# Optimization experiments

Measured on AMD Instinct MI355X. Metric: run time of the kernel, lower is better.

The kernel has to match this reference:

```python
import jax, jax.numpy as jnp
import numpy as np
import math

HEAD_NUM = 16


def _split_qkv(qkv, head_num):
    # torch: rearrange(qkv, 'b t (d k h) -> k b h t d', k=3, h=head_num)
    B, T, E3 = qkv.shape
    d = E3 // (3 * head_num)
    qkv = qkv.reshape(B, T, d, 3, head_num)        # (b,t,d,k,h)
    qkv = jnp.transpose(qkv, (3, 0, 4, 1, 2))       # (k,b,h,t,d)
    return qkv[0], qkv[1], qkv[2]


def setup_inputs() -> dict:
    key = jax.random.key(0)
    ks = jax.random.split(key, 6)
    B, T, E = 4, 1024, 1024
    return {
        "x": jax.random.normal(ks[0], (B, T, E), dtype=jnp.float32),
        "y": jax.random.normal(ks[1], (B, T, E), dtype=jnp.float32),
        "Wqkv1": jax.random.normal(ks[2], (3 * E, E), dtype=jnp.float32) * 0.02,
        "Wqkv2": jax.random.normal(ks[3], (3 * E, E), dtype=jnp.float32) * 0.02,
        "Wout1": jax.random.normal(ks[4], (E, E), dtype=jnp.float32) * 0.02,
        "Wout2": jax.random.normal(ks[5], (E, E), dtype=jnp.float32) * 0.02,
    }


def reference(x, y, Wqkv1, Wqkv2, Wout1, Wout2):
    B, T, E = x.shape
    H = HEAD_NUM
    dk = math.sqrt(E / H)

    qkv1 = x @ Wqkv1.T                              # (B,T,3E)
    qkv2 = y @ Wqkv2.T
    q1, k1, v1 = _split_qkv(qkv1, H)                # each (B,H,T,d)
    q2, k2, v2 = _split_qkv(qkv2, H)

    # cross attention: stream-2 queries attend to stream-1 keys/values and vice versa
    energy1 = jnp.einsum('bhid,bhjd->bhij', q2, k1) / dk
    energy2 = jnp.einsum('bhid,bhjd->bhij', q1, k2) / dk
    attn1 = jax.nn.softmax(energy1, axis=-1)
    attn2 = jax.nn.softmax(energy2, axis=-1)

    xo = jnp.einsum('bhij,bhjd->bhid', attn1, v1)   # (B,H,T,d)
    yo = jnp.einsum('bhij,bhjd->bhid', attn2, v2)
    xo = jnp.transpose(xo, (0, 2, 1, 3)).reshape(B, T, E)  # b t (h d)
    yo = jnp.transpose(yo, (0, 2, 1, 3)).reshape(B, T, E)

    return xo @ Wout1.T, yo @ Wout2.T
```

## Files before the change

kernel.cpp:

```cpp
#include <hip/hip_runtime.h>
#include <hip/hip_bf16.h>

typedef __hip_bfloat16 bf16;
typedef __attribute__((ext_vector_type(8))) short short8;
typedef __attribute__((ext_vector_type(4))) short short4v;
typedef __attribute__((ext_vector_type(4))) float f32x4;

#define MFMA_BF16(a, b, c) __builtin_amdgcn_mfma_f32_16x16x32_bf16((a), (b), (c), 0, 0, 0)

#define QSCALE 0.1803368860111270f

__device__ __forceinline__ short f2bf(float f) {
    union { bf16 h; short s; } u;
    u.h = __float2bfloat16(f);
    return u.s;
}

#if defined(__has_builtin) && __has_builtin(__builtin_amdgcn_cvt_pk_bf16_f32)
typedef __attribute__((ext_vector_type(2))) __bf16 bf16x2_t;
__device__ __forceinline__ unsigned int pk2(float a, float b) {
    union { bf16x2_t v; unsigned int u; } x;
    x.v = __builtin_amdgcn_cvt_pk_bf16_f32(a, b);
    return x.u;
}
#else
__device__ __forceinline__ unsigned int pk2(float a, float b) {
    union { bf16 h[2]; unsigned int u; } x;
    x.h[0] = __float2bfloat16(a);
    x.h[1] = __float2bfloat16(b);
    return x.u;
}
#endif

#if defined(__has_builtin) && __has_builtin(__builtin_amdgcn_exp2f)
#define EXP2F(x) __builtin_amdgcn_exp2f(x)
#else
#define EXP2F(x) exp2f(x)
#endif

__device__ __forceinline__ void gload16(const void* g, void* l) {
    __builtin_amdgcn_global_load_lds(
        (const __attribute__((address_space(1))) unsigned int*)g,
        (__attribute__((address_space(3))) unsigned int*)l, 16, 0, 0);
}

__global__ void cvt_fused(const float* __restrict__ x, const float* __restrict__ y,
                          const float* __restrict__ wo1, const float* __restrict__ wo2,
                          const float* __restrict__ wq1, const float* __restrict__ wq2,
                          bf16* __restrict__ ox, bf16* __restrict__ oy,
                          bf16* __restrict__ oo1, bf16* __restrict__ oo2,
                          bf16* __restrict__ oq1, bf16* __restrict__ oq2) {
    const int yb = blockIdx.y;
    if (yb < 4) {
        int i = blockIdx.x * 256 + threadIdx.x;
        const float* src; bf16* dst; int n4;
        switch (yb) {
            case 0:  src = x;   dst = ox;  n4 = 1048576; break;
            case 1:  src = y;   dst = oy;  n4 = 1048576; break;
            case 2:  src = wo1; dst = oo1; n4 = 262144;  break;
            default: src = wo2; dst = oo2; n4 = 262144;  break;
        }
        if (i >= n4) return;
        float4 f = reinterpret_cast<const float4*>(src)[i];
        short4v s;
        s.x = f2bf(f.x); s.y = f2bf(f.y); s.z = f2bf(f.z); s.w = f2bf(f.w);
        reinterpret_cast<short4v*>(dst)[i] = s;
    } else {
        const int np = blockIdx.x;
        if (np >= 3072) return;
        const int comp = np >> 10, rem = np & 1023, h = rem >> 6, d = rem & 63;
        const int srow = d * 48 + comp * 16 + h;
        const float* src = ((yb == 5) ? wq2 : wq1) + (long)srow * 1024;
        bf16* dst = ((yb == 5) ? oq2 : oq1) + (long)np * 1024;
        const float sc = (comp == 0) ? QSCALE : 1.0f;
        int t = threadIdx.x;
        float4 f = reinterpret_cast<const float4*>(src)[t];
        short4v s;
        s.x = f2bf(f.x * sc); s.y = f2bf(f.y * sc); s.z = f2bf(f.z * sc); s.w = f2bf(f.w * sc);
        reinterpret_cast<short4v*>(dst)[t] = s;
    }
}

__global__ __launch_bounds__(512, 4)
void gemm_qkv128(const bf16* __restrict__ A0g, const bf16* __restrict__ B0g,
                 void* o0a, void* o0b, void* o0c,
                 const bf16* __restrict__ A1g, const bf16* __restrict__ B1g,
                 void* o1a, void* o1b, void* o1c) {
    extern __shared__ short smem[];
    const int z = blockIdx.z;
    const short* A = reinterpret_cast<const short*>(z ? A1g : A0g);
    const short* B = reinterpret_cast<const short*>(z ? B1g : B0g);
    const int tid  = threadIdx.x;
    const int lane = tid & 63;
    const int w    = tid >> 6;
    const int quad = lane >> 4;
    const int l16  = lane & 15;
    const long M0 = (long)blockIdx.y * 128;
    const long N0 = (long)blockIdx.x * 256;

    const int wm = w >> 2;
    const int wn = w & 3;
    const int cA0  = (quad ^ ((l16 >> 1) & 3)) * 8;
    const int aoff = wm * 2048 + l16 * 32;
    const int boff = 4096 + wn * 1024 + l16 * 32;

    const int srow = lane >> 2;
    const int scs  = ((lane & 3) ^ ((srow >> 1) & 3)) * 8;
    const short* Asrc = A + (M0 + 16 * w + srow) * 1024 + scs;
    const short* Bsrc = B + (N0 + 32 * w + srow) * 1024 + scs;

    f32x4 acc[2][4][2] = {};
    short8 af[4], bfv[2];

#define SA128(tt, nbase) do { \
    gload16(Asrc + (tt) * 32, smem + (nbase) + w * 512); } while (0)
#define SB128(tt, nbase) do { \
    const short* _s = Bsrc + (tt) * 32; \
    short* _d = smem + (nbase) + 4096 + w * 1024; \
    gload16(_s, _d); gload16(_s + 16384, _d + 512); } while (0)
#define RDA128(bbv) do { \
    _Pragma("unroll") for (int mt = 0; mt < 4; ++mt) \
        af[mt] = *reinterpret_cast<const short8*>(&smem[(bbv) + aoff + mt * 512 + cA0]); } while (0)
#define RDB128(Bh, bbv) do { \
    _Pragma("unroll") for (int nt = 0; nt < 2; ++nt) \
        bfv[nt] = *reinterpret_cast<const short8*>(&smem[(bbv) + (Bh) * 4096 + boff + nt * 512 + cA0]); } while (0)
#define MM128(p) do { \
    __builtin_amdgcn_s_setprio(1); \
    _Pragma("unroll") for (int mt = 0; mt < 4; ++mt) \
    _Pragma("unroll") for (int nt = 0; nt < 2; ++nt) \
        acc[p][mt][nt] = MFMA_BF16(af[mt], bfv[nt], acc[p][mt][nt]); \
    __builtin_amdgcn_s_setprio(0); } while (0)

    SA128(0, 0); SB128(0, 0);

    int bcur = 0;
#pragma unroll 1
    for (int t = 0; t < 32; ++t) {
        int bnext = bcur + 1; if (bnext == 3) bnext = 0;
        if (t < 31) {
            const int nb = bnext * 12288;
            SA128(t + 1, nb); SB128(t + 1, nb);
            asm volatile("s_waitcnt vmcnt(3)" ::: "memory");
        } else {
            asm volatile("s_waitcnt vmcnt(0)" ::: "memory");
        }
        __builtin_amdgcn_s_barrier();
        __builtin_amdgcn_sched_barrier(0);

        const int bb = bcur * 12288;
        RDA128(bb);
        RDB128(0, bb);
        MM128(0);
        RDB128(1, bb);
        MM128(1);
        bcur = bnext;
    }

    __syncthreads();

    if (blockIdx.x < 8) {
        short* dst = reinterpret_cast<short*>(blockIdx.x < 4 ? (z ? o1a : o0a)
                                                             : (z ? o1b : o0b));
        const int b = (int)(M0 >> 10);
        const int t00 = ((int)M0 & 1023) + wm * 64 + quad * 4;
        const int hd00 = ((int)blockIdx.x & 3) * 256 + wn * 32;
#pragma unroll
        for (int Bh = 0; Bh < 2; ++Bh)
#pragma unroll
            for (int nt = 0; nt < 2; ++nt) {
                const int hd = hd00 + Bh * 128 + nt * 16 + l16;
                const int h = hd >> 6, d = hd & 63;
                short* dp = dst + (long)(b * 16 + h) * 65536 + d;
#pragma unroll
                for (int mt = 0; mt < 4; ++mt)
#pragma unroll
                    for (int r = 0; r < 4; ++r)
                        dp[(long)(t00 + mt * 16 + r) * 64] = f2bf(acc[Bh][mt][nt][r]);
            }
    } else {
        short* vT = reinterpret_cast<short*>(z ? o1c : o0c);
        const int b = (int)(M0 >> 10);
        const int hd00 = ((int)blockIdx.x - 8) * 256 + wn * 32;
        short* ws = smem + w * 2304;
        const int c8 = (lane & 7) * 8;
        const int colr = lane >> 3;
        const int tb = ((int)M0 & 1023) + wm * 64 + c8;
#pragma unroll
        for (int Bh = 0; Bh < 2; ++Bh) {
#pragma unroll
            for (int nt = 0; nt < 2; ++nt)
#pragma unroll
                for (int mt = 0; mt < 4; ++mt) {
                    uint2 uu;
                    uu.x = pk2(acc[Bh][mt][nt][0], acc[Bh][mt][nt][1]);
                    uu.y = pk2(acc[Bh][mt][nt][2], acc[Bh][mt][nt][3]);
                    *reinterpret_cast<uint2*>(&ws[(nt * 16 + l16) * 72 + mt * 16 + quad * 4]) = uu;
                }
#pragma unroll
            for (int q4 = 0; q4 < 4; ++q4) {
                const int col = q4 * 8 + colr;
                const int hd = hd00 + Bh * 128 + col;
                const int h = hd >> 6, d = hd & 63;
                short8 v = *reinterpret_cast<const short8*>(&ws[col * 72 + c8]);
                *reinterpret_cast<short8*>(&vT[(long)(b * 16 + h) * 65536 + (long)d * 1024 + tb]) = v;
            }
        }
    }
#undef SA128
#undef SB128
#undef RDA128
#undef RDB128
#undef MM128
}

__global__ __launch_bounds__(256)
void gemm_out(const bf16* __restrict__ A0g, const bf16* __restrict__ B0g, float* __restrict__ C0,
              const bf16* __restrict__ A1g, const bf16* __restrict__ B1g, float* __restrict__ C1) {
    __shared__ short smem2[24576];
    const int z = blockIdx.z;
    const short* A = reinterpret_cast<const short*>(z ? A1g : A0g);
    const short* B = reinterpret_cast<const short*>(z ? B1g : B0g);
    const int tid  = threadIdx.x;
    const int lane = tid & 63;
    const int w    = tid >> 6;
    const int wr   = w >> 1;
    const int wc   = w & 1;
    const int quad = lane >> 4;
    const int l16  = lane & 15;
    const long bM = (long)blockIdx.y * 128;

    f32x4 acc[4][4] = {};

    const int sr  = lane >> 2;
    const int scs = ((lane & 3) ^ (sr & 3)) * 8;
    const short* Ag0 = A + (bM + 32 * w + sr) * 1024 + scs;
    const short* Ag1 = Ag0 + 16 * 1024;
    const short* Bg0 = B + ((long)blockIdx.x * 128 + 32 * w + sr) * 1024 + scs;
    const short* Bg1 = Bg0 + 16 * 1024;
    const int sq = (quad ^ (l16 & 3)) * 8;

    {
        short* sb = smem2;
        gload16(Ag0, sb + w * 1024);
        gload16(Ag1, sb + w * 1024 + 512);
        gload16(Bg0, sb + 4096 + w * 1024);
        gload16(Bg1, sb + 4096 + w * 1024 + 512);
    }

    int bcur = 0;
#pragma unroll 1
    for (int iter = 0; iter < 32; ++iter) {
        int bnext = bcur + 1; if (bnext == 3) bnext = 0;
        if (iter < 31) {
            const int koff = (iter + 1) * 32;
            short* sb = smem2 + bnext * 8192;
            gload16(Ag0 + koff, sb + w * 1024);
            gload16(Ag1 + koff, sb + w * 1024 + 512);
            gload16(Bg0 + koff, sb + 4096 + w * 1024);
            gload16(Bg1 + koff, sb + 4096 + w * 1024 + 512);
            asm volatile("s_waitcnt vmcnt(4)" ::: "memory");
        } else {
            asm volatile("s_waitcnt vmcnt(0)" ::: "memory");
        }
        __builtin_amdgcn_s_barrier();
        __builtin_amdgcn_sched_barrier(0);

        const short* Ab = smem2 + bcur * 8192;
        const short* Bb = Ab + 4096;

        short8 af[4], bfr[4];
#pragma unroll
        for (int mt = 0; mt < 4; ++mt)
            af[mt] = *reinterpret_cast<const short8*>(&Ab[(wr * 64 + mt * 16 + l16) * 32 + sq]);
#pragma unroll
        for (int nt = 0; nt < 4; ++nt)
            bfr[nt] = *reinterpret_cast<const short8*>(&Bb[(wc * 64 + nt * 16 + l16) * 32 + sq]);
        __builtin_amdgcn_s_setprio(1);
#pragma unroll
        for (int mt = 0; mt < 4; ++mt)
#pragma unroll
            for (int nt = 0; nt < 4; ++nt)
                acc[mt][nt] = MFMA_BF16(af[mt], bfr[nt], acc[mt][nt]);
        __builtin_amdgcn_s_setprio(0);
        bcur = bnext;
    }

    float* C = z ? C1 : C0;
    const long crow = bM + wr * 64 + quad * 4;
    const long ccol = (long)blockIdx.x * 128 + wc * 64 + l16;
#pragma unroll
    for (int mt = 0; mt < 4; ++mt)
#pragma unroll
        for (int nt = 0; nt < 4; ++nt)
#pragma unroll
            for (int r = 0; r < 4; ++r)
                C[(crow + mt * 16 + r) * 1024L + ccol + nt * 16] = acc[mt][nt][r];
}

__global__ __launch_bounds__(256)
void attn_kernel(const bf16* __restrict__ q0g, const bf16* __restrict__ k0g,
                 const bf16* __restrict__ v0g, bf16* __restrict__ o0g,
                 const bf16* __restrict__ q1g, const bf16* __restrict__ k1g,
                 const bf16* __restrict__ v1g, bf16* __restrict__ o1g) {
    __shared__ short smem[24576];
    const int bh = blockIdx.x;
    const int qt = blockIdx.y;
    const int z = blockIdx.z;
    const int b = bh >> 4, h = bh & 15;
    const int tid = threadIdx.x, lane = tid & 63, w = tid >> 6;
    const int quad = lane >> 4, l16 = lane & 15;

    const short* Qb = reinterpret_cast<const short*>(z ? q1g : q0g) + (long)bh * 1024 * 64;
    const short* Kb = reinterpret_cast<const short*>(z ? k1g : k0g) + (long)bh * 1024 * 64;
    const short* Vb = reinterpret_cast<const short*>(z ? v1g : v0g) + (long)bh * 64 * 1024;
    short* Ob = reinterpret_cast<short*>(z ? o1g : o0g);

    short8 qb[2][2];
#pragma unroll
    for (int qg = 0; qg < 2; ++qg) {
        const short* Qp = Qb + (long)(qt * 128 + qg * 64 + w * 16 + l16) * 64;
        qb[qg][0] = *reinterpret_cast<const short8*>(Qp + quad * 8);
        qb[qg][1] = *reinterpret_cast<const short8*>(Qp + 32 + quad * 8);
    }

    const int r8  = lane >> 3;
    const int sc0 = ((lane & 7) ^ (r8 & 3)) * 8;
    const short* Kg0 = Kb + (long)(16 * w + r8) * 64 + sc0;
    const short* Kg1 = Kb + (long)(16 * w + 8 + r8) * 64 + (sc0 ^ 32);
    const short* Vg0 = Vb + (long)(16 * w + r8) * 1024 + sc0;
    const short* Vg1 = Vb + (long)(16 * w + 8 + r8) * 1024 + (sc0 ^ 32);

    const int jbase = 8 * (l16 >> 2) + (l16 & 3);
    const int fKs = (l16 & 3) | (((l16 >> 2) & 1) << 2);
    const int s0  = (quad ^ fKs) * 8;
    const int fVs = (l16 & 3) | (((l16 >> 3) & 1) << 2);
    const int sv  = (quad ^ fVs) * 8;

    f32x4 o[2][4] = {};
    float li[2] = {0.f, 0.f};

    gload16(Kg0, smem + w * 1024); gload16(Kg1, smem + w * 1024 + 512);
    gload16(Vg0, smem + 4096 + w * 1024); gload16(Vg1, smem + 4096 + w * 1024 + 512);

    int bcur = 0;
#pragma unroll 1
    for (int iter = 0; iter < 16; ++iter) {
        int bnext = bcur + 1; if (bnext == 3) bnext = 0;
        if (iter < 15) {
            short* sb = smem + bnext * 8192;
            const long ko = (long)(iter + 1) * 4096;
            const long vo = (long)(iter + 1) * 64;
            gload16(Kg0 + ko, sb + w * 1024);
            gload16(Kg1 + ko, sb + w * 1024 + 512);
            gload16(Vg0 + vo, sb + 4096 + w * 1024);
            gload16(Vg1 + vo, sb + 4096 + w * 1024 + 512);
            asm volatile("s_waitcnt vmcnt(4)" ::: "memory");
        } else {
            asm volatile("s_waitcnt vmcnt(0)" ::: "memory");
        }
        __builtin_amdgcn_s_barrier();
        __builtin_amdgcn_sched_barrier(0);

        const short* Ks = smem + bcur * 8192;
        const short* Vs = Ks + 4096;

        f32x4 st[2][4];
        __builtin_amdgcn_s_setprio(1);
#pragma unroll
        for (int g = 0; g < 4; ++g) {
            const int goff = (g >> 1) * 32 + (g & 1) * 4;
            const short* kr = Ks + (jbase + goff) * 64;
            short8 k0 = *reinterpret_cast<const short8*>(kr + s0);
            short8 k1 = *reinterpret_cast<const short8*>(kr + (s0 ^ 32));
#pragma unroll
            for (int qg = 0; qg < 2; ++qg) {
                f32x4 zf = {0.f, 0.f, 0.f, 0.f};
                zf = MFMA_BF16(k0, qb[qg][0], zf);
                zf = MFMA_BF16(k1, qb[qg][1], zf);
                st[qg][g] = zf;
            }
        }
        __builtin_amdgcn_s_setprio(0);

        union { unsigned int u[4]; short8 s; } f0[2], f1[2];
#pragma unroll
        for (int qg = 0; qg < 2; ++qg) {
            float p[4][4];
            float rs = 0.f;
#pragma unroll
            for (int g = 0; g < 4; ++g)
#pragma unroll
                for (int r = 0; r < 4; ++r) {
                    float e = EXP2F(st[qg][g][r]);
                    p[g][r] = e;
                    rs += e;
                }
            li[qg] += rs;
            f0[qg].u[0] = pk2(p[0][0], p[0][1]); f0[qg].u[1] = pk2(p[0][2], p[0][3]);
            f0[qg].u[2] = pk2(p[1][0], p[1][1]); f0[qg].u[3] = pk2(p[1][2], p[1][3]);
            f1[qg].u[0] = pk2(p[2][0], p[2][1]); f1[qg].u[1] = pk2(p[2][2], p[2][3]);
            f1[qg].u[2] = pk2(p[3][0], p[3][1]); f1[qg].u[3] = pk2(p[3][2], p[3][3]);
        }

        __builtin_amdgcn_s_setprio(1);
#pragma unroll
        for (int dt = 0; dt < 4; ++dt) {
            const short* vr = Vs + (dt * 16 + l16) * 64;
            short8 v0 = *reinterpret_cast<const short8*>(vr + sv);
            short8 v1 = *reinterpret_cast<const short8*>(vr + (sv ^ 32));
#pragma unroll
            for (int qg = 0; qg < 2; ++qg) {
                o[qg][dt] = MFMA_BF16(v0, f0[qg].s, o[qg][dt]);
                o[qg][dt] = MFMA_BF16(v1, f1[qg].s, o[qg][dt]);
            }
        }
        __builtin_amdgcn_s_setprio(0);
        bcur = bnext;
    }

    __syncthreads();

#pragma unroll
    for (int qg = 0; qg < 2; ++qg) {
        li[qg] += __shfl_xor(li[qg], 16);
        li[qg] += __shfl_xor(li[qg], 32);
    }

#pragma unroll
    for (int qg = 0; qg < 2; ++qg) {
        short* Os = smem + qg * 5120 + w * 1280;
        const float rl = 1.0f / li[qg];
#pragma unroll
        for (int dt = 0; dt < 4; ++dt) {
            uint2 uu;
            uu.x = pk2(o[qg][dt][0] * rl, o[qg][dt][1] * rl);
            uu.y = pk2(o[qg][dt][2] * rl, o[qg][dt][3] * rl);
            *reinterpret_cast<uint2*>(&Os[l16 * 80 + dt * 16 + quad * 4]) = uu;
        }
#pragma unroll
        for (int p = 0; p < 2; ++p) {
            int row = p * 8 + (lane >> 3);
            int ch = (lane & 7) * 8;
            short8 v = *reinterpret_cast<const short8*>(&Os[row * 80 + ch]);
            *reinterpret_cast<short8*>(&Ob[((long)(b * 1024) + qt * 128 + qg * 64 + w * 16 + row) * 1024 + h * 64 + ch]) = v;
        }
    }
}

extern "C" void kernel_launch(void* const* d_in, const int* in_sizes, int n_in,
                              void* d_out, int out_size, void* d_ws, size_t ws_size,
                              hipStream_t stream) {
    const float* x     = (const float*)d_in[0];
    const float* y     = (const float*)d_in[1];
    const float* Wqkv1 = (const float*)d_in[2];
    const float* Wqkv2 = (const float*)d_in[3];
    const float* Wout1 = (const float*)d_in[4];
    const float* Wout2 = (const float*)d_in[5];

    char* ws = (char*)d_ws;
    bf16* Wqkv1b = (bf16*)(ws + 0);
    bf16* Wqkv2b = (bf16*)(ws + 6291456);
    bf16* Wout1b = (bf16*)(ws + 12582912);
    bf16* Wout2b = (bf16*)(ws + 14680064);
    bf16* xb     = (bf16*)(ws + 16777216);
    bf16* yb     = (bf16*)(ws + 25165824);
    bf16* q1     = (bf16*)(ws + 33554432);
    bf16* k1     = (bf16*)(ws + 41943040);
    bf16* v1T    = (bf16*)(ws + 50331648);
    bf16* q2     = (bf16*)(ws + 58720256);
    bf16* k2     = (bf16*)(ws + 67108864);
    bf16* v2T    = (bf16*)(ws + 75497472);
    bf16* xo     = xb;
    bf16* yo     = yb;

    static bool s_attr = false;
    if (!s_attr) {
        (void)hipFuncSetAttribute(reinterpret_cast<const void*>(&gemm_qkv128),
                                  hipFuncAttributeMaxDynamicSharedMemorySize, 73728);
        s_attr = true;
    }

    cvt_fused<<<dim3(4096, 6), 256, 0, stream>>>(x, y, Wout1, Wout2, Wqkv1, Wqkv2,
                                                 xb, yb, Wout1b, Wout2b, Wqkv1b, Wqkv2b);

    gemm_qkv128<<<dim3(12, 32, 2), 512, 73728, stream>>>(xb, Wqkv1b, q1, k1, v1T,
                                                         yb, Wqkv2b, q2, k2, v2T);

    attn_kernel<<<dim3(64, 8, 2), 256, 0, stream>>>(q2, k1, v1T, xo,
                                                    q1, k2, v2T, yo);

    gemm_out<<<dim3(8, 32, 2), 256, 0, stream>>>(xo, Wout1b, (float*)d_out,
                                                 yo, Wout2b, ((float*)d_out) + 4194304);
}
```

Before: 240.6 us.

## Enlarge QKV GEMM tile to 256x256 with double-buffered LDS pipeline

```diff
diff --git a/kernel.cpp b/kernel.cpp
--- a/kernel.cpp
+++ b/kernel.cpp
@@ -82,7 +82,7 @@
 }
 
 __global__ __launch_bounds__(512, 4)
-void gemm_qkv128(const bf16* __restrict__ A0g, const bf16* __restrict__ B0g,
+void gemm_qkv256(const bf16* __restrict__ A0g, const bf16* __restrict__ B0g,
                  void* o0a, void* o0b, void* o0c,
                  const bf16* __restrict__ A1g, const bf16* __restrict__ B1g,
                  void* o1a, void* o1b, void* o1c) {
@@ -95,65 +95,53 @@
     const int w    = tid >> 6;
     const int quad = lane >> 4;
     const int l16  = lane & 15;
-    const long M0 = (long)blockIdx.y * 128;
+    const long M0 = (long)blockIdx.y * 256;
     const long N0 = (long)blockIdx.x * 256;
 
     const int wm = w >> 2;
     const int wn = w & 3;
     const int cA0  = (quad ^ ((l16 >> 1) & 3)) * 8;
-    const int aoff = wm * 2048 + l16 * 32;
-    const int boff = 4096 + wn * 1024 + l16 * 32;
+    const int aoff = wm * 4096 + l16 * 32;
+    const int boff = 8192 + wn * 2048 + l16 * 32;
 
     const int srow = lane >> 2;
     const int scs  = ((lane & 3) ^ ((srow >> 1) & 3)) * 8;
-    const short* Asrc = A + (M0 + 16 * w + srow) * 1024 + scs;
+    const short* Asrc = A + (M0 + 32 * w + srow) * 1024 + scs;
     const short* Bsrc = B + (N0 + 32 * w + srow) * 1024 + scs;
 
-    f32x4 acc[2][4][2] = {};
-    short8 af[4], bfv[2];
-
-#define SA128(tt, nbase) do { \
-    gload16(Asrc + (tt) * 32, smem + (nbase) + w * 512); } while (0)
-#define SB128(tt, nbase) do { \
-    const short* _s = Bsrc + (tt) * 32; \
-    short* _d = smem + (nbase) + 4096 + w * 1024; \
-    gload16(_s, _d); gload16(_s + 16384, _d + 512); } while (0)
-#define RDA128(bbv) do { \
-    _Pragma("unroll") for (int mt = 0; mt < 4; ++mt) \
-        af[mt] = *reinterpret_cast<const short8*>(&smem[(bbv) + aoff + mt * 512 + cA0]); } while (0)
-#define RDB128(Bh, bbv) do { \
-    _Pragma("unroll") for (int nt = 0; nt < 2; ++nt) \
-        bfv[nt] = *reinterpret_cast<const short8*>(&smem[(bbv) + (Bh) * 4096 + boff + nt * 512 + cA0]); } while (0)
-#define MM128(p) do { \
+    f32x4 acc[8][4] = {};
+    short8 af[8], bfv[4];
+
+#define STG(tt, nbase) do { \
+    const short* _a = Asrc + (tt) * 32; \
+    const short* _b = Bsrc + (tt) * 32; \
+    short* _da = smem + (nbase) + w * 1024; \
+    short* _db = _da + 8192; \
+    gload16(_a, _da); gload16(_a + 16384, _da + 512); \
+    gload16(_b, _db); gload16(_b + 16384, _db + 512); } while (0)
+#define RDALL(bbv) do { \
+    _Pragma("unroll") for (int mt = 0; mt < 8; ++mt) \
+        af[mt] = *reinterpret_cast<const short8*>(&smem[(bbv) + aoff + mt * 512 + cA0]); \
+    _Pragma("unroll") for (int nt = 0; nt < 4; ++nt) \
+        bfv[nt] = *reinterpret_cast<const short8*>(&smem[(bbv) + boff + nt * 512 + cA0]); } while (0)
+#define MMALL() do { \
     __builtin_amdgcn_s_setprio(1); \
-    _Pragma("unroll") for (int mt = 0; mt < 4; ++mt) \
-    _Pragma("unroll") for (int nt = 0; nt < 2; ++nt) \
-        acc[p][mt][nt] = MFMA_BF16(af[mt], bfv[nt], acc[p][mt][nt]); \
+    _Pragma("unroll") for (int mt = 0; mt < 8; ++mt) \
+    _Pragma("unroll") for (int nt = 0; nt < 4; ++nt) \
+        acc[mt][nt] = MFMA_BF16(af[mt], bfv[nt], acc[mt][nt]); \
     __builtin_amdgcn_s_setprio(0); } while (0)
 
-    SA128(0, 0); SB128(0, 0);
-
-    int bcur = 0;
+    STG(0, 0);
+
 #pragma unroll 1
     for (int t = 0; t < 32; ++t) {
-        int bnext = bcur + 1; if (bnext == 3) bnext = 0;
-        if (t < 31) {
-            const int nb = bnext * 12288;
-            SA128(t + 1, nb); SB128(t + 1, nb);
-            asm volatile("s_waitcnt vmcnt(3)" ::: "memory");
-        } else {
-            asm volatile("s_waitcnt vmcnt(0)" ::: "memory");
-        }
+        asm volatile("s_waitcnt vmcnt(0)" ::: "memory");
         __builtin_amdgcn_s_barrier();
         __builtin_amdgcn_sched_barrier(0);
-
-        const int bb = bcur * 12288;
-        RDA128(bb);
-        RDB128(0, bb);
-        MM128(0);
-        RDB128(1, bb);
-        MM128(1);
-        bcur = bnext;
+        if (t < 31) STG(t + 1, ((t + 1) & 1) << 14);
+        const int bb = (t & 1) << 14;
+        RDALL(bb);
+        MMALL();
     }
 
     __syncthreads();
@@ -162,55 +150,53 @@
         short* dst = reinterpret_cast<short*>(blockIdx.x < 4 ? (z ? o1a : o0a)
                                                              : (z ? o1b : o0b));
         const int b = (int)(M0 >> 10);
-        const int t00 = ((int)M0 & 1023) + wm * 64 + quad * 4;
-        const int hd00 = ((int)blockIdx.x & 3) * 256 + wn * 32;
-#pragma unroll
-        for (int Bh = 0; Bh < 2; ++Bh)
-#pragma unroll
-            for (int nt = 0; nt < 2; ++nt) {
-                const int hd = hd00 + Bh * 128 + nt * 16 + l16;
-                const int h = hd >> 6, d = hd & 63;
-                short* dp = dst + (long)(b * 16 + h) * 65536 + d;
-#pragma unroll
-                for (int mt = 0; mt < 4; ++mt)
-#pragma unroll
-                    for (int r = 0; r < 4; ++r)
-                        dp[(long)(t00 + mt * 16 + r) * 64] = f2bf(acc[Bh][mt][nt][r]);
-            }
+        const int t00 = ((int)M0 & 1023) + wm * 128 + quad * 4;
+        const int hd00 = ((int)blockIdx.x & 3) * 256 + wn * 64;
+#pragma unroll
+        for (int nt = 0; nt < 4; ++nt) {
+            const int hd = hd00 + nt * 16 + l16;
+            const int h = hd >> 6, d = hd & 63;
+            short* dp = dst + (long)(b * 16 + h) * 65536 + d;
+#pragma unroll
+            for (int mt = 0; mt < 8; ++mt)
+#pragma unroll
+                for (int r = 0; r < 4; ++r)
+                    dp[(long)(t00 + mt * 16 + r) * 64] = f2bf(acc[mt][nt][r]);
+        }
     } else {
         short* vT = reinterpret_cast<short*>(z ? o1c : o0c);
         const int b = (int)(M0 >> 10);
-        const int hd00 = ((int)blockIdx.x - 8) * 256 + wn * 32;
         short* ws = smem + w * 2304;
         const int c8 = (lane & 7) * 8;
         const int colr = lane >> 3;
-        const int tb = ((int)M0 & 1023) + wm * 64 + c8;
-#pragma unroll
-        for (int Bh = 0; Bh < 2; ++Bh) {
-#pragma unroll
-            for (int nt = 0; nt < 2; ++nt)
-#pragma unroll
-                for (int mt = 0; mt < 4; ++mt) {
+#pragma unroll
+        for (int ph = 0; ph < 4; ++ph) {
+            const int mh = ph >> 1, np = ph & 1;
+#pragma unroll
+            for (int ntl = 0; ntl < 2; ++ntl)
+#pragma unroll
+                for (int mtl = 0; mtl < 4; ++mtl) {
+                    const f32x4 a = acc[mh * 4 + mtl][np * 2 + ntl];
                     uint2 uu;
-                    uu.x = pk2(acc[Bh][mt][nt][0], acc[Bh][mt][nt][1]);
-                    uu.y = pk2(acc[Bh][mt][nt][2], acc[Bh][mt][nt][3]);
-                    *reinterpret_cast<uint2*>(&ws[(nt * 16 + l16) * 72 + mt * 16 + quad * 4]) = uu;
+                    uu.x = pk2(a[0], a[1]);
+                    uu.y = pk2(a[2], a[3]);
+                    *reinterpret_cast<uint2*>(&ws[(ntl * 16 + l16) * 72 + mtl * 16 + quad * 4]) = uu;
                 }
+            const int tb = ((int)M0 & 1023) + wm * 128 + mh * 64 + c8;
+            const int hd00v = ((int)blockIdx.x - 8) * 256 + wn * 64 + np * 32;
 #pragma unroll
             for (int q4 = 0; q4 < 4; ++q4) {
                 const int col = q4 * 8 + colr;
-                const int hd = hd00 + Bh * 128 + col;
+                const int hd = hd00v + col;
                 const int h = hd >> 6, d = hd & 63;
                 short8 v = *reinterpret_cast<const short8*>(&ws[col * 72 + c8]);
                 *reinterpret_cast<short8*>(&vT[(long)(b * 16 + h) * 65536 + (long)d * 1024 + tb]) = v;
             }
         }
     }
-#undef SA128
-#undef SB128
-#undef RDA128
-#undef RDB128
-#undef MM128
+#undef STG
+#undef RDALL
+#undef MMALL
 }
 
 __global__ __launch_bounds__(256)
@@ -475,15 +461,15 @@
 
     static bool s_attr = false;
     if (!s_attr) {
-        (void)hipFuncSetAttribute(reinterpret_cast<const void*>(&gemm_qkv128),
-                                  hipFuncAttributeMaxDynamicSharedMemorySize, 73728);
+        (void)hipFuncSetAttribute(reinterpret_cast<const void*>(&gemm_qkv256),
+                                  hipFuncAttributeMaxDynamicSharedMemorySize, 65536);
         s_attr = true;
     }
 
     cvt_fused<<<dim3(4096, 6), 256, 0, stream>>>(x, y, Wout1, Wout2, Wqkv1, Wqkv2,
                                                  xb, yb, Wout1b, Wout2b, Wqkv1b, Wqkv2b);
 
-    gemm_qkv128<<<dim3(12, 32, 2), 512, 73728, stream>>>(xb, Wqkv1b, q1, k1, v1T,
+    gemm_qkv256<<<dim3(12, 16, 2), 512, 65536, stream>>>(xb, Wqkv1b, q1, k1, v1T,
                                                          yb, Wqkv2b, q2, k2, v2T);
 
     attn_kernel<<<dim3(64, 8, 2), 256, 0, stream>>>(q2, k1, v1T, xo,
```

Measured after the change: 697.9 us. 190% more time.
